# Kernel tuning notes

Hardware: AMD Instinct MI355X
Metric: run time of the kernel (lower is better)

Reference implementation:

```python
import jax, jax.numpy as jnp
import numpy as np

NUM_PTS = 1024
LATENT_SIZE = 32
BETA = 0.1


def setup_inputs() -> dict:
    key = jax.random.key(0)
    k1, k2, k3, k4 = jax.random.split(key, 4)
    B = 128
    return {
        "recon_x": jax.random.normal(k1, (B, NUM_PTS, 3), dtype=jnp.float32),
        "x": jax.random.normal(k2, (B, NUM_PTS, 3), dtype=jnp.float32),
        "mu": jax.random.normal(k3, (B, LATENT_SIZE), dtype=jnp.float32),
        "logvar": jax.random.normal(k4, (B, LATENT_SIZE), dtype=jnp.float32),
    }


def _chamfer(recon_x, x):
    # Batched squared pairwise distances: P[b, i, j] = ||x[b,i] - recon_x[b,j]||^2
    xx = jnp.sum(x * x, axis=-1)              # [B, N]
    yy = jnp.sum(recon_x * recon_x, axis=-1)  # [B, N]
    xy = jnp.einsum("bnd,bmd->bnm", x, recon_x)  # [B, N, N]
    P = xx[:, :, None] + yy[:, None, :] - 2.0 * xy
    # Bidirectional min + sum
    loss_1 = jnp.sum(jnp.min(P, axis=1))  # for each recon point, nearest x point
    loss_2 = jnp.sum(jnp.min(P, axis=2))  # for each x point, nearest recon point
    return loss_1 + loss_2


def reference(recon_x, x, mu, logvar):
    RE = _chamfer(recon_x, x) / NUM_PTS
    KLD = -0.5 * jnp.sum(1.0 + logvar - mu * mu - jnp.exp(logvar))
    KLD = KLD / LATENT_SIZE
    return RE + KLD * BETA
```

## Files before the change

### kernel.cpp

```cpp
#include <hip/hip_runtime.h>

#define NUM_PTS 1024
#define NBATCH 128
#define BT 128
#define RT 256
#define NJC 16
#define JC 64
#define R 16
#define CHAMF_SCALE (1.0f / 1024.0f)
#define KLD_SCALE   (-0.5f * 0.1f / 32.0f)

#define WS_CHUNK (NBATCH * NUM_PTS)
#define WS_DIR   (NJC * WS_CHUNK)

__global__ __launch_bounds__(BT, 4) void chamfer_part(
    const float* __restrict__ recon_x,
    const float* __restrict__ x,
    float* __restrict__ ws)
{
    const int b  = blockIdx.x >> 4;
    const int c  = blockIdx.x & 15;
    const int w  = threadIdx.x >> 6;
    const int lt = threadIdx.x & 63;

    __shared__ float sq[2][4][JC];
    {
        const float* qsrc = (w == 0 ? recon_x : x)
                            + (size_t)b * NUM_PTS * 3 + (size_t)c * JC * 3 + 3 * lt;
        const float qx = qsrc[0], qy = qsrc[1], qz = qsrc[2];
        sq[w][0][lt] = qx;
        sq[w][1][lt] = qy;
        sq[w][2][lt] = qz;
        sq[w][3][lt] = fmaf(qx, qx, fmaf(qy, qy, qz * qz));
    }

    const float* rp = (w == 0 ? x : recon_x) + (size_t)b * NUM_PTS * 3;
    float vx[R], vy[R], vz[R], m[R];
    {
        const float4* __restrict__ s4 = (const float4*)(rp + 48 * lt);
        float buf[48];
        float4* bp = (float4*)buf;
#pragma unroll
        for (int i = 0; i < 12; ++i) bp[i] = s4[i];
#pragma unroll
        for (int k = 0; k < R; ++k) {
            vx[k] = -2.0f * buf[3 * k + 0];
            vy[k] = -2.0f * buf[3 * k + 1];
            vz[k] = -2.0f * buf[3 * k + 2];
            m[k]  = 1e30f;
        }
    }
    __syncthreads();

    const float4* __restrict__ qxp = (const float4*)sq[w][0];
    const float4* __restrict__ qyp = (const float4*)sq[w][1];
    const float4* __restrict__ qzp = (const float4*)sq[w][2];
    const float4* __restrict__ q2p = (const float4*)sq[w][3];
#pragma unroll 2
    for (int g = 0; g < JC / 4; ++g) {
        const float4 qx = qxp[g];
        const float4 qy = qyp[g];
        const float4 qz = qzp[g];
        const float4 q2 = q2p[g];
#pragma unroll
        for (int r = 0; r < R; ++r) {
            const float d0 = fmaf(vx[r], qx.x, fmaf(vy[r], qy.x, fmaf(vz[r], qz.x, q2.x)));
            const float d1 = fmaf(vx[r], qx.y, fmaf(vy[r], qy.y, fmaf(vz[r], qz.y, q2.y)));
            m[r] = fminf(fminf(m[r], d0), d1);
        }
#pragma unroll
        for (int r = 0; r < R; ++r) {
            const float d2 = fmaf(vx[r], qx.z, fmaf(vy[r], qy.z, fmaf(vz[r], qz.z, q2.z)));
            const float d3 = fmaf(vx[r], qx.w, fmaf(vy[r], qy.w, fmaf(vz[r], qz.w, q2.w)));
            m[r] = fminf(fminf(m[r], d2), d3);
        }
    }

    float4* dst = (float4*)(ws + (size_t)w * WS_DIR + (size_t)c * WS_CHUNK
                            + b * NUM_PTS + 16 * lt);
#pragma unroll
    for (int k4 = 0; k4 < 4; ++k4) {
        float o[4];
#pragma unroll
        for (int i = 0; i < 4; ++i) {
            const int k = 4 * k4 + i;
            const float r2 = 0.25f * fmaf(vx[k], vx[k], fmaf(vy[k], vy[k], vz[k] * vz[k]));
            o[i] = r2 + m[k];
        }
        dst[k4] = make_float4(o[0], o[1], o[2], o[3]);
    }
}

__global__ __launch_bounds__(RT) void reduce_kernel(
    const float* __restrict__ ws,
    const float* __restrict__ mu,
    const float* __restrict__ logvar,
    float* __restrict__ out)
{
    const int gid  = blockIdx.x * RT + threadIdx.x;
    const int base = gid * 4;
    const int dir  = base >> 17;
    const int rem  = base & 131071;

    const float4* p = (const float4*)(ws + (size_t)dir * WS_DIR + rem);
    float4 mn = p[0];
#pragma unroll
    for (int c = 1; c < NJC; ++c) {
        const float4 q = p[c * (WS_CHUNK / 4)];
        mn.x = fminf(mn.x, q.x);
        mn.y = fminf(mn.y, q.y);
        mn.z = fminf(mn.z, q.z);
        mn.w = fminf(mn.w, q.w);
    }
    float v = (mn.x + mn.y + mn.z + mn.w) * CHAMF_SCALE;

    if (blockIdx.x < 16) {
        const int t = blockIdx.x * RT + threadIdx.x;
        const float lv = logvar[t];
        const float mm = mu[t];
        v += (1.0f + lv - mm * mm - expf(lv)) * KLD_SCALE;
    }

    for (int off = 32; off > 0; off >>= 1)
        v += __shfl_down(v, off, 64);

    __shared__ float red[RT / 64];
    const int lane = threadIdx.x & 63;
    const int wv   = threadIdx.x >> 6;
    if (lane == 0) red[wv] = v;
    __syncthreads();
    if (threadIdx.x == 0) {
        float sum = 0.f;
        for (int wq = 0; wq < RT / 64; ++wq) sum += red[wq];
        atomicAdd(out, sum);
    }
}

extern "C" void kernel_launch(void* const* d_in, const int* in_sizes, int n_in,
                              void* d_out, int out_size, void* d_ws, size_t ws_size,
                              hipStream_t stream) {
    const float* recon_x = (const float*)d_in[0];
    const float* x       = (const float*)d_in[1];
    const float* mu      = (const float*)d_in[2];
    const float* logvar  = (const float*)d_in[3];
    float* out = (float*)d_out;
    float* ws  = (float*)d_ws;

    (void)hipMemsetAsync(out, 0, sizeof(float), stream);

    chamfer_part<<<NBATCH * NJC, BT, 0, stream>>>(recon_x, x, ws);
    reduce_kernel<<<256, RT, 0, stream>>>(ws, mu, logvar, out);
}
```

Before: 93.86 us.

## Merge two query chunks per block via LDS to halve workspace partial-min traffic

Each block now has four wavefronts: two directions times two 64-query halves. The two halves are merged by taking a min through shared memory before writing, so the number of partial-min chunks drops from 16 to 8. This halves the workspace writes in the chamfer kernel and the reads in the reduce kernel. The batch/chunk block-index mapping is swapped, and the block-wide barrier after loading queries is removed because each wave reads only its own LDS slice. The launch-bounds target is now 256 threads with 4 blocks per CU, which tightens the register budget and may cause spills.

After: 89.09 us. 5.1% less time.

```diff
diff --git a/kernel.cpp b/kernel.cpp
--- a/kernel.cpp
+++ b/kernel.cpp
@@ -2,10 +2,10 @@
 
 #define NUM_PTS 1024
 #define NBATCH 128
-#define BT 128
+#define BT 256
 #define RT 256
-#define NJC 16
-#define JC 64
+#define NJC 8
+#define JCH 64
 #define R 16
 #define CHAMF_SCALE (1.0f / 1024.0f)
 #define KLD_SCALE   (-0.5f * 0.1f / 32.0f)
@@ -18,15 +18,19 @@
     const float* __restrict__ x,
     float* __restrict__ ws)
 {
-    const int b  = blockIdx.x >> 4;
-    const int c  = blockIdx.x & 15;
+    const int b  = blockIdx.x & 127;
+    const int c  = blockIdx.x >> 7;
     const int w  = threadIdx.x >> 6;
     const int lt = threadIdx.x & 63;
+    const int dir  = w & 1;
+    const int half = w >> 1;
 
-    __shared__ float sq[2][4][JC];
+    __shared__ float sq[4][4][JCH];
+    __shared__ float comb[2][NUM_PTS + 64];
+
     {
-        const float* qsrc = (w == 0 ? recon_x : x)
-                            + (size_t)b * NUM_PTS * 3 + (size_t)c * JC * 3 + 3 * lt;
+        const float* qsrc = (dir == 0 ? recon_x : x)
+            + (size_t)b * NUM_PTS * 3 + (size_t)(c * 128 + half * JCH + lt) * 3;
         const float qx = qsrc[0], qy = qsrc[1], qz = qsrc[2];
         sq[w][0][lt] = qx;
         sq[w][1][lt] = qy;
@@ -34,11 +38,11 @@
         sq[w][3][lt] = fmaf(qx, qx, fmaf(qy, qy, qz * qz));
     }
 
-    const float* rp = (w == 0 ? x : recon_x) + (size_t)b * NUM_PTS * 3;
+    const float* rp = (dir == 0 ? x : recon_x) + (size_t)b * NUM_PTS * 3;
     float vx[R], vy[R], vz[R], m[R];
     {
+        float buf[48];
         const float4* __restrict__ s4 = (const float4*)(rp + 48 * lt);
-        float buf[48];
         float4* bp = (float4*)buf;
 #pragma unroll
         for (int i = 0; i < 12; ++i) bp[i] = s4[i];
@@ -50,14 +54,13 @@
             m[k]  = 1e30f;
         }
     }
-    __syncthreads();
 
     const float4* __restrict__ qxp = (const float4*)sq[w][0];
     const float4* __restrict__ qyp = (const float4*)sq[w][1];
     const float4* __restrict__ qzp = (const float4*)sq[w][2];
     const float4* __restrict__ q2p = (const float4*)sq[w][3];
 #pragma unroll 2
-    for (int g = 0; g < JC / 4; ++g) {
+    for (int g = 0; g < JCH / 4; ++g) {
         const float4 qx = qxp[g];
         const float4 qy = qyp[g];
         const float4 qz = qzp[g];
@@ -76,18 +79,28 @@
         }
     }
 
-    float4* dst = (float4*)(ws + (size_t)w * WS_DIR + (size_t)c * WS_CHUNK
-                            + b * NUM_PTS + 16 * lt);
+    if (half == 0) {
 #pragma unroll
-    for (int k4 = 0; k4 < 4; ++k4) {
-        float o[4];
+        for (int k = 0; k < R; ++k)
+            comb[dir][17 * lt + k] = m[k];
+    }
+    __syncthreads();
+    if (half == 1) {
+        float4* dst = (float4*)(ws + (size_t)dir * WS_DIR + (size_t)c * WS_CHUNK
+                                + b * NUM_PTS + 16 * lt);
 #pragma unroll
-        for (int i = 0; i < 4; ++i) {
-            const int k = 4 * k4 + i;
-            const float r2 = 0.25f * fmaf(vx[k], vx[k], fmaf(vy[k], vy[k], vz[k] * vz[k]));
-            o[i] = r2 + m[k];
+        for (int k4 = 0; k4 < 4; ++k4) {
+            float o[4];
+#pragma unroll
+            for (int i = 0; i < 4; ++i) {
+                const int k = 4 * k4 + i;
+                const float mm = fminf(m[k], comb[dir][17 * lt + k]);
+                const float r2 = 0.25f * fmaf(vx[k], vx[k],
+                                        fmaf(vy[k], vy[k], vz[k] * vz[k]));
+                o[i] = r2 + mm;
+            }
+            dst[k4] = make_float4(o[0], o[1], o[2], o[3]);
         }
-        dst[k4] = make_float4(o[0], o[1], o[2], o[3]);
     }
 }
 
```
